# Kernel tuning notes

Measured on AMD Instinct MI355X. Metric: run time of the kernel, lower is better.

Reference implementation:

```python
import jax, jax.numpy as jnp
import numpy as np

B, S, H, NH = 8, 1024, 1024, 16
DH = H // NH


def setup_inputs() -> dict:
    key = jax.random.key(0)
    ks = jax.random.split(key, 16)
    inp = {
        'v': jax.random.normal(ks[0], (B, S, H), jnp.float32),
        'k': jax.random.normal(ks[1], (B, S, H), jnp.float32),
        'q': jax.random.normal(ks[2], (B, S, H), jnp.float32),
        'r': jax.random.normal(ks[3], (B, S, H), jnp.float32),
        'mask': jax.random.randint(ks[4], (B, 1, 1, S), 0, 2).astype(jnp.bool_),
    }
    scale = 1.0 / np.sqrt(H)
    names = ['Wv', 'Wk', 'Wq', 'Wr', 'Wm']
    for i, n in enumerate(names):
        inp[n] = jax.random.normal(ks[5 + i], (H, H), jnp.float32) * scale
        inp['b' + n[1:]] = jnp.zeros((H,), jnp.float32)
    return inp


def _heads(x, W, b):
    # torch Linear: x @ W.T + b, then split heads -> [B, NH, S, DH]
    y = jnp.einsum('bsh,oh->bso', x, W) + b
    return y.reshape(B, S, NH, DH).transpose(0, 2, 1, 3)


def reference(v, k, q, r, mask, Wv, bv, Wk, bk, Wq, bq, Wr, br, Wm, bm):
    vh = _heads(v, Wv, bv)
    kh = _heads(k, Wk, bk)
    qh = _heads(q, Wq, bq)
    rh = _heads(r, Wr, br)
    # relation-augmented scores: (QK^T + RK^T) / sqrt(d_k)
    scores = jnp.einsum('bhqd,bhkd->bhqk', qh + rh, kh) / jnp.sqrt(jnp.asarray(DH, qh.dtype))
    scores = jnp.where(mask, jnp.asarray(-1e9, scores.dtype), scores)
    att = jax.nn.softmax(scores, axis=-1)  # dropout = identity in eval
    out = jnp.einsum('bhqk,bhkd->bhqd', att, vh)
    out = out.transpose(0, 2, 1, 3).reshape(B, S, H)
    return jnp.einsum('bsh,oh->bso', out, Wm) + bm
```

## Files before the change

kernel.cpp:

```cpp
#include <hip/hip_runtime.h>
#include <hip/hip_bf16.h>
#include <stdint.h>

typedef __attribute__((ext_vector_type(4))) float f32x4;
typedef __attribute__((ext_vector_type(8))) short s16x8;
typedef __attribute__((ext_vector_type(4))) short s16x4;

typedef const __attribute__((address_space(1))) unsigned glb_u32;
typedef __attribute__((address_space(3))) unsigned lds_u32;

#define DEVI __device__ __forceinline__

DEVI short f2b(float f) {
    union { float f; unsigned u; } v; v.f = f;
    unsigned r = v.u + 0x7fffu + ((v.u >> 16) & 1u);
    return (short)(r >> 16);
}

struct Ptr5 { const float* p[5]; };
struct Ptr4 { const float* p[4]; };

__global__ __launch_bounds__(256) void cvtW(Ptr5 src, short* __restrict__ dst) {
    const float* s = src.p[blockIdx.y];
    short* d = dst + (size_t)blockIdx.y * (1024u * 1024u);
    int i = (blockIdx.x * 256 + threadIdx.x) * 8;
    f32x4 a = *(const f32x4*)(s + i);
    f32x4 b = *(const f32x4*)(s + i + 4);
    s16x8 o;
#pragma unroll
    for (int j = 0; j < 4; ++j) { o[j] = f2b(a[j]); o[4 + j] = f2b(b[j]); }
    *(s16x8*)(d + i) = o;
}

__global__ __launch_bounds__(256) void cvtA(Ptr4 src, short* __restrict__ dst) {
    const float* s = src.p[blockIdx.y];
    short* d = dst + (size_t)blockIdx.y * (8u * 1024u * 1024u);
    int i = (blockIdx.x * 256 + threadIdx.x) * 8;
    f32x4 a = *(const f32x4*)(s + i);
    f32x4 b = *(const f32x4*)(s + i + 4);
    s16x8 o;
#pragma unroll
    for (int j = 0; j < 4; ++j) { o[j] = f2b(a[j]); o[4 + j] = f2b(b[j]); }
    *(s16x8*)(d + i) = o;
}

template<int AF32, int OUTMODE, int TWO>
__global__ __launch_bounds__(256) void gemm_nt(
    const void* __restrict__ A0_, const void* __restrict__ A1_,
    const short* __restrict__ W0, const short* __restrict__ W1,
    const float* __restrict__ b0, const float* __restrict__ b1,
    void* __restrict__ C_)
{
    constexpr int K = 1024, N = 1024;
    const int tid = threadIdx.x;
    const int lane = tid & 63, wid = tid >> 6;
    const int wm = wid >> 1, wn = wid & 1;
    const int r = lane & 15, g = lane >> 4;

    const int bid = blockIdx.x;
    const int logical = (bid & 7) * 64 + (bid >> 3);
    const int n0 = (logical & 7) * 128, m0 = (logical >> 3) * 128;

    __shared__ alignas(16) short As[2][128 * 32];
    __shared__ alignas(16) short Ws[2][128 * 32];

    auto stage_async = [&](int buf, int kt) {
        int kk = kt * 32;
        const short* Ap = (const short*)A0_; const short* Wp = W0;
        if (TWO && kk >= 1024) { Ap = (const short*)A1_; Wp = W1; kk &= 1023; }
#pragma unroll
        for (int i = 0; i < 2; ++i) {
            int row = wid * 32 + i * 16 + (lane >> 2);
            const short* ga = Ap + (size_t)(m0 + row) * K + kk + (lane & 3) * 8;
            const short* gw = Wp + (size_t)(n0 + row) * K + kk + (lane & 3) * 8;
            __builtin_amdgcn_global_load_lds((glb_u32*)ga,
                (lds_u32*)&As[buf][(wid * 32 + i * 16) * 32], 16, 0, 0);
            __builtin_amdgcn_global_load_lds((glb_u32*)gw,
                (lds_u32*)&Ws[buf][(wid * 32 + i * 16) * 32], 16, 0, 0);
        }
    };

    const int srow = tid >> 1, shalf = tid & 1;
    f32x4 a0g, a1g, a2g, a3g;
    s16x8 wg0, wg1;
    auto load_regs = [&](int kt) {
        int kk = kt * 32;
        const short* wp = W0 + (size_t)(n0 + srow) * K + kk + shalf * 16;
        wg0 = *(const s16x8*)wp;
        wg1 = *(const s16x8*)(wp + 8);
        const float* ap = (const float*)A0_ + (size_t)(m0 + srow) * K + kk + shalf * 16;
        a0g = *(const f32x4*)ap;       a1g = *(const f32x4*)(ap + 4);
        a2g = *(const f32x4*)(ap + 8); a3g = *(const f32x4*)(ap + 12);
    };
    auto store_lds = [&](int buf) {
        s16x8 s0, s1;
#pragma unroll
        for (int j = 0; j < 4; ++j) {
            s0[j] = f2b(a0g[j]); s0[4 + j] = f2b(a1g[j]);
            s1[j] = f2b(a2g[j]); s1[4 + j] = f2b(a3g[j]);
        }
        char* ab = (char*)As[buf];
        *(s16x8*)(ab + srow * 64 + shalf * 32) = s0;
        *(s16x8*)(ab + srow * 64 + shalf * 32 + 16) = s1;
        char* wb = (char*)Ws[buf];
        *(s16x8*)(wb + srow * 64 + shalf * 32) = wg0;
        *(s16x8*)(wb + srow * 64 + shalf * 32 + 16) = wg1;
    };

    f32x4 z = {0.f, 0.f, 0.f, 0.f};
    f32x4 acc[4][4];
#pragma unroll
    for (int i = 0; i < 4; ++i)
#pragma unroll
        for (int j = 0; j < 4; ++j) acc[i][j] = z;

    auto compute = [&](int buf) {
        s16x8 af[4], bfr[4];
#pragma unroll
        for (int f = 0; f < 4; ++f) {
            af[f]  = *(const s16x8*)&As[buf][(wm * 64 + f * 16 + r) * 32 + g * 8];
            bfr[f] = *(const s16x8*)&Ws[buf][(wn * 64 + f * 16 + r) * 32 + g * 8];
        }
#pragma unroll
        for (int i = 0; i < 4; ++i)
#pragma unroll
            for (int j = 0; j < 4; ++j)
                acc[i][j] = __builtin_amdgcn_mfma_f32_16x16x32_bf16(af[i], bfr[j], acc[i][j], 0, 0, 0);
    };

    constexpr int NK = TWO ? 64 : 32;
    if constexpr (AF32) { load_regs(0); store_lds(0); }
    else stage_async(0, 0);
    __syncthreads();
    int buf = 0;
    for (int kt = 0; kt < NK; ++kt) {
        if (kt + 1 < NK) {
            if constexpr (AF32) load_regs(kt + 1);
            else stage_async(buf ^ 1, kt + 1);
        }
        compute(buf);
        if (AF32 && kt + 1 < NK) store_lds(buf ^ 1);
        __syncthreads();
        buf ^= 1;
    }

#pragma unroll
    for (int j = 0; j < 4; ++j) {
        int col = n0 + wn * 64 + j * 16 + r;
        float bb = b0[col];
        if (TWO) bb += b1[col];
#pragma unroll
        for (int i = 0; i < 4; ++i) {
            int rowb = m0 + wm * 64 + i * 16 + g * 4;
            if constexpr (OUTMODE == 2) {
                int bb_ = rowb >> 10, tok = rowb & 1023;
                short* dst = (short*)C_ + ((size_t)(bb_ * 16 + (col >> 6))) * 65536
                           + (size_t)(col & 63) * 1024 + tok;
                s16x4 o;
#pragma unroll
                for (int q = 0; q < 4; ++q) o[q] = f2b(acc[i][j][q] + bb);
                *(s16x4*)dst = o;
            } else {
#pragma unroll
                for (int q = 0; q < 4; ++q) {
                    float val = acc[i][j][q] + bb;
                    if constexpr (OUTMODE == 1)
                        ((float*)C_)[(size_t)(rowb + q) * N + col] = val;
                    else
                        ((short*)C_)[(size_t)(rowb + q) * N + col] = f2b(val);
                }
            }
        }
    }
}

__global__ __launch_bounds__(256) void attn_fwd(
    const short* __restrict__ qrh, const short* __restrict__ kh,
    const short* __restrict__ vT, const int* __restrict__ mask,
    short* __restrict__ outp)
{
    const int bh = blockIdx.x;
    const int b = bh >> 4, h = bh & 15;
    const int qt = blockIdx.y;
    const int tid = threadIdx.x, lane = tid & 63, wid = tid >> 6;
    const int r = lane & 15, g = lane >> 4;

    __shared__ alignas(16) short Ks[64 * 64];
    __shared__ alignas(16) short Vs[64 * 64];
    __shared__ alignas(16) float mb[64];

    const int q0 = qt * 64 + wid * 16;
    const short* qbase = qrh + (size_t)(b * 1024 + q0 + r) * 1024 + h * 64;
    s16x8 qf0 = *(const s16x8*)(qbase + g * 8);
    s16x8 qf1 = *(const s16x8*)(qbase + 32 + g * 8);

    f32x4 z = {0.f, 0.f, 0.f, 0.f};
    f32x4 oacc[4];
#pragma unroll
    for (int i = 0; i < 4; ++i) oacc[i] = z;
    float mrun = -1e30f, lrun = 0.f;

    const int srow = tid >> 2, sq = tid & 3;
    const short* kg = kh + (size_t)(b * 1024 + srow) * 1024 + h * 64 + sq * 16;
    const short* vg = vT + ((size_t)(b * 16 + h)) * 65536 + (size_t)srow * 1024 + sq * 16;
    const int p0s = (sq * 2) ^ (srow & 7), p1s = (sq * 2 + 1) ^ (srow & 7);

    for (int t = 0; t < 16; ++t) {
        const int k0 = t * 64;
        if (t) __syncthreads();
        {
            const short* kp = kg + (size_t)k0 * 1024;
            s16x8 k0v = *(const s16x8*)kp;
            s16x8 k1v = *(const s16x8*)(kp + 8);
            char* kb = (char*)Ks;
            *(s16x8*)(kb + srow * 128 + p0s * 16) = k0v;
            *(s16x8*)(kb + srow * 128 + p1s * 16) = k1v;
        }
        {
            const short* vp = vg + k0;
            s16x8 v0 = *(const s16x8*)vp;
            s16x8 v1 = *(const s16x8*)(vp + 8);
            char* vb = (char*)Vs;
            *(s16x8*)(vb + srow * 128 + p0s * 16) = v0;
            *(s16x8*)(vb + srow * 128 + p1s * 16) = v1;
        }
        if (tid < 64) mb[tid] = mask[b * 1024 + k0 + tid] ? -1e9f : 0.f;
        __syncthreads();

        float p[4][4];
        float tmax = -3e38f;
#pragma unroll
        for (int fn = 0; fn < 4; ++fn) {
            int row = fn * 16 + r;
            char* kb = (char*)Ks;
            s16x8 kfa = *(const s16x8*)(kb + row * 128 + ((g ^ (row & 7)) << 4));
            s16x8 kfb = *(const s16x8*)(kb + row * 128 + (((4 + g) ^ (row & 7)) << 4));
            f32x4 c = __builtin_amdgcn_mfma_f32_16x16x32_bf16(kfa, qf0, z, 0, 0, 0);
            c = __builtin_amdgcn_mfma_f32_16x16x32_bf16(kfb, qf1, c, 0, 0, 0);
            f32x4 mv = *(const f32x4*)&mb[fn * 16 + g * 4];
#pragma unroll
            for (int qi = 0; qi < 4; ++qi) {
                float s = c[qi] * 0.125f + mv[qi];
                p[fn][qi] = s;
                tmax = fmaxf(tmax, s);
            }
        }
        tmax = fmaxf(tmax, __shfl_xor(tmax, 16));
        tmax = fmaxf(tmax, __shfl_xor(tmax, 32));

        float mn = fmaxf(mrun, tmax);
        float corr = __expf(mrun - mn);
        mrun = mn;
        float tsum = 0.f;
#pragma unroll
        for (int fn = 0; fn < 4; ++fn)
#pragma unroll
            for (int qi = 0; qi < 4; ++qi) {
                float e = __expf(p[fn][qi] - mn);
                p[fn][qi] = e;
                tsum += e;
            }
        tsum += __shfl_xor(tsum, 16);
        tsum += __shfl_xor(tsum, 32);
        lrun = lrun * corr + tsum;
#pragma unroll
        for (int df = 0; df < 4; ++df)
#pragma unroll
            for (int qi = 0; qi < 4; ++qi) oacc[df][qi] *= corr;

#pragma unroll
        for (int ks = 0; ks < 2; ++ks) {
            s16x8 pb;
#pragma unroll
            for (int j = 0; j < 4; ++j) {
                pb[j]     = f2b(p[2 * ks][j]);
                pb[4 + j] = f2b(p[2 * ks + 1][j]);
            }
#pragma unroll
            for (int df = 0; df < 4; ++df) {
                int row = df * 16 + r;
                int sl0 = ks * 4 + (g >> 1), half = (g & 1) * 8;
                char* vb = (char*)Vs;
                s16x4 va0 = *(const s16x4*)(vb + row * 128 + ((sl0 ^ (row & 7)) << 4) + half);
                s16x4 va1 = *(const s16x4*)(vb + row * 128 + (((sl0 + 2) ^ (row & 7)) << 4) + half);
                s16x8 vf = {va0[0], va0[1], va0[2], va0[3], va1[0], va1[1], va1[2], va1[3]};
                oacc[df] = __builtin_amdgcn_mfma_f32_16x16x32_bf16(vf, pb, oacc[df], 0, 0, 0);
            }
        }
    }

    float inv = 1.f / lrun;
#pragma unroll
    for (int df = 0; df < 4; ++df) {
        s16x4 o;
#pragma unroll
        for (int qi = 0; qi < 4; ++qi) o[qi] = f2b(oacc[df][qi] * inv);
        *(s16x4*)&outp[(size_t)(b * 1024 + q0 + r) * 1024 + h * 64 + df * 16 + g * 4] = o;
    }
}

extern "C" void kernel_launch(void* const* d_in, const int* in_sizes, int n_in,
                              void* d_out, int out_size, void* d_ws, size_t ws_size,
                              hipStream_t stream) {
    const float* v  = (const float*)d_in[0];
    const float* k  = (const float*)d_in[1];
    const float* q  = (const float*)d_in[2];
    const float* rr = (const float*)d_in[3];
    const int* mask = (const int*)d_in[4];
    const float* Wv = (const float*)d_in[5];  const float* bv = (const float*)d_in[6];
    const float* Wk = (const float*)d_in[7];  const float* bk = (const float*)d_in[8];
    const float* Wq = (const float*)d_in[9];  const float* bq = (const float*)d_in[10];
    const float* Wr = (const float*)d_in[11]; const float* br = (const float*)d_in[12];
    const float* Wm = (const float*)d_in[13]; const float* bm = (const float*)d_in[14];

    const size_t MB = 1048576u;
    const size_t NEED_FULL = 90u * MB;
    const size_t NEED_B    = 74u * MB;
    char* ws = (char*)d_ws;
    short* Wb = (short*)ws;

    Ptr5 p5;
    p5.p[0] = Wv; p5.p[1] = Wk; p5.p[2] = Wq; p5.p[3] = Wr; p5.p[4] = Wm;
    cvtW<<<dim3(512, 5), 256, 0, stream>>>(p5, Wb);

    const short* Wvb = Wb, *Wkb = Wb + 1048576u, *Wqb = Wb + 2097152u,
               *Wrb = Wb + 3145728u, *Wmb = Wb + 4194304u;
    dim3 gg(512);

    if (ws_size >= NEED_FULL) {
        short* vb  = (short*)(ws + 10u * MB);
        short* kb  = vb + 8388608u;
        short* qb  = kb + 8388608u;
        short* rb  = qb + 8388608u;
        short* vtb = rb + 8388608u;
        short* khb = vb;
        short* qrb = kb;
        short* att = qb;

        Ptr4 p4; p4.p[0] = v; p4.p[1] = k; p4.p[2] = q; p4.p[3] = rr;
        cvtA<<<dim3(4096, 4), 256, 0, stream>>>(p4, vb);

        gemm_nt<0, 2, 0><<<gg, 256, 0, stream>>>(vb, nullptr, Wvb, nullptr, bv, nullptr, vtb);
        gemm_nt<0, 0, 0><<<gg, 256, 0, stream>>>(kb, nullptr, Wkb, nullptr, bk, nullptr, khb);
        gemm_nt<0, 0, 1><<<gg, 256, 0, stream>>>(qb, rb, Wqb, Wrb, bq, br, qrb);
        attn_fwd<<<dim3(128, 16), 256, 0, stream>>>(qrb, khb, vtb, mask, att);
        gemm_nt<0, 1, 0><<<gg, 256, 0, stream>>>(att, nullptr, Wmb, nullptr, bm, nullptr, (float*)d_out);
    } else if (ws_size >= NEED_B) {
        short* kb  = (short*)(ws + 10u * MB);
        short* qb  = kb + 8388608u;
        short* rb  = qb + 8388608u;
        short* qrb = rb + 8388608u;
        short* vtb = qb;
        short* khb = rb;
        short* att = kb;

        Ptr4 p4; p4.p[0] = k; p4.p[1] = q; p4.p[2] = rr; p4.p[3] = k;
        cvtA<<<dim3(4096, 3), 256, 0, stream>>>(p4, kb);

        gemm_nt<0, 0, 1><<<gg, 256, 0, stream>>>(qb, rb, Wqb, Wrb, bq, br, qrb);
        gemm_nt<1, 2, 0><<<gg, 256, 0, stream>>>(v, nullptr, Wvb, nullptr, bv, nullptr, vtb);
        gemm_nt<0, 0, 0><<<gg, 256, 0, stream>>>(kb, nullptr, Wkb, nullptr, bk, nullptr, khb);
        attn_fwd<<<dim3(128, 16), 256, 0, stream>>>(qrb, khb, vtb, mask, att);
        gemm_nt<0, 1, 0><<<gg, 256, 0, stream>>>(att, nullptr, Wmb, nullptr, bm, nullptr, (float*)d_out);
    }
}
```

Baseline: 261.1 us.

## Process two query tiles per wave, prefetch K/V tiles, preload full mask

Each wave now handles 32 query rows (two 16-row sub-tiles) so every K and V fragment read from LDS feeds two MFMAs, halving K/V global and LDS traffic per query. The next K/V tile is loaded into registers while the current tile is computed, overlapping global latency with compute. The per-row mask is converted once into a 1024-entry LDS array instead of once per tile. The attention grid is halved to 128x8 blocks, which raises register pressure and lowers the number of blocks available to fill the GPU.

Measured after the change: 253.3 us. 3.0% less time.

```diff
diff --git a/kernel.cpp b/kernel.cpp
--- a/kernel.cpp
+++ b/kernel.cpp
@@ -5,6 +5,7 @@
 typedef __attribute__((ext_vector_type(4))) float f32x4;
 typedef __attribute__((ext_vector_type(8))) short s16x8;
 typedef __attribute__((ext_vector_type(4))) short s16x4;
+typedef __attribute__((ext_vector_type(4))) int i32x4;
 
 typedef const __attribute__((address_space(1))) unsigned glb_u32;
 typedef __attribute__((address_space(3))) unsigned lds_u32;
@@ -187,115 +188,136 @@
 
     __shared__ alignas(16) short Ks[64 * 64];
     __shared__ alignas(16) short Vs[64 * 64];
-    __shared__ alignas(16) float mb[64];
-
-    const int q0 = qt * 64 + wid * 16;
-    const short* qbase = qrh + (size_t)(b * 1024 + q0 + r) * 1024 + h * 64;
-    s16x8 qf0 = *(const s16x8*)(qbase + g * 8);
-    s16x8 qf1 = *(const s16x8*)(qbase + 32 + g * 8);
+    __shared__ alignas(16) float mb[1024];
+
+    {
+        i32x4 mi = *(const i32x4*)(mask + b * 1024 + tid * 4);
+        f32x4 mv;
+#pragma unroll
+        for (int j = 0; j < 4; ++j) mv[j] = mi[j] ? -1e9f : 0.f;
+        *(f32x4*)&mb[tid * 4] = mv;
+    }
+
+    const int q0 = qt * 128 + wid * 32;
+    const short* qbA = qrh + (size_t)(b * 1024 + q0 + r) * 1024 + h * 64;
+    const short* qbB = qbA + 16 * 1024;
+    s16x8 qA0 = *(const s16x8*)(qbA + g * 8);
+    s16x8 qA1 = *(const s16x8*)(qbA + 32 + g * 8);
+    s16x8 qB0 = *(const s16x8*)(qbB + g * 8);
+    s16x8 qB1 = *(const s16x8*)(qbB + 32 + g * 8);
 
     f32x4 z = {0.f, 0.f, 0.f, 0.f};
-    f32x4 oacc[4];
-#pragma unroll
-    for (int i = 0; i < 4; ++i) oacc[i] = z;
-    float mrun = -1e30f, lrun = 0.f;
+    f32x4 oA[4], oB[4];
+#pragma unroll
+    for (int i = 0; i < 4; ++i) { oA[i] = z; oB[i] = z; }
+    float mA = -1e30f, mB = -1e30f, lA = 0.f, lB = 0.f;
 
     const int srow = tid >> 2, sq = tid & 3;
     const short* kg = kh + (size_t)(b * 1024 + srow) * 1024 + h * 64 + sq * 16;
     const short* vg = vT + ((size_t)(b * 16 + h)) * 65536 + (size_t)srow * 1024 + sq * 16;
     const int p0s = (sq * 2) ^ (srow & 7), p1s = (sq * 2 + 1) ^ (srow & 7);
 
+    s16x8 kr0, kr1, vr0, vr1;
+    auto stage_load = [&](int t) {
+        const short* kp = kg + (size_t)(t * 64) * 1024;
+        kr0 = *(const s16x8*)kp; kr1 = *(const s16x8*)(kp + 8);
+        const short* vp = vg + t * 64;
+        vr0 = *(const s16x8*)vp; vr1 = *(const s16x8*)(vp + 8);
+    };
+    auto stage_write = [&]() {
+        char* kb2 = (char*)Ks;
+        *(s16x8*)(kb2 + srow * 128 + p0s * 16) = kr0;
+        *(s16x8*)(kb2 + srow * 128 + p1s * 16) = kr1;
+        char* vb2 = (char*)Vs;
+        *(s16x8*)(vb2 + srow * 128 + p0s * 16) = vr0;
+        *(s16x8*)(vb2 + srow * 128 + p1s * 16) = vr1;
+    };
+
+    stage_load(0);
     for (int t = 0; t < 16; ++t) {
-        const int k0 = t * 64;
         if (t) __syncthreads();
-        {
-            const short* kp = kg + (size_t)k0 * 1024;
-            s16x8 k0v = *(const s16x8*)kp;
-            s16x8 k1v = *(const s16x8*)(kp + 8);
-            char* kb = (char*)Ks;
-            *(s16x8*)(kb + srow * 128 + p0s * 16) = k0v;
-            *(s16x8*)(kb + srow * 128 + p1s * 16) = k1v;
-        }
-        {
-            const short* vp = vg + k0;
-            s16x8 v0 = *(const s16x8*)vp;
-            s16x8 v1 = *(const s16x8*)(vp + 8);
-            char* vb = (char*)Vs;
-            *(s16x8*)(vb + srow * 128 + p0s * 16) = v0;
-            *(s16x8*)(vb + srow * 128 + p1s * 16) = v1;
-        }
-        if (tid < 64) mb[tid] = mask[b * 1024 + k0 + tid] ? -1e9f : 0.f;
+        stage_write();
         __syncthreads();
-
-        float p[4][4];
-        float tmax = -3e38f;
+        if (t < 15) stage_load(t + 1);
+
+        f32x4 pA[4], pB[4];
+        float tmA = -3e38f, tmB = -3e38f;
+        char* kb2 = (char*)Ks;
 #pragma unroll
         for (int fn = 0; fn < 4; ++fn) {
             int row = fn * 16 + r;
-            char* kb = (char*)Ks;
-            s16x8 kfa = *(const s16x8*)(kb + row * 128 + ((g ^ (row & 7)) << 4));
-            s16x8 kfb = *(const s16x8*)(kb + row * 128 + (((4 + g) ^ (row & 7)) << 4));
-            f32x4 c = __builtin_amdgcn_mfma_f32_16x16x32_bf16(kfa, qf0, z, 0, 0, 0);
-            c = __builtin_amdgcn_mfma_f32_16x16x32_bf16(kfb, qf1, c, 0, 0, 0);
-            f32x4 mv = *(const f32x4*)&mb[fn * 16 + g * 4];
+            s16x8 kfa = *(const s16x8*)(kb2 + row * 128 + ((g ^ (row & 7)) << 4));
+            s16x8 kfb = *(const s16x8*)(kb2 + row * 128 + (((4 + g) ^ (row & 7)) << 4));
+            f32x4 cA = __builtin_amdgcn_mfma_f32_16x16x32_bf16(kfa, qA0, z, 0, 0, 0);
+            cA = __builtin_amdgcn_mfma_f32_16x16x32_bf16(kfb, qA1, cA, 0, 0, 0);
+            f32x4 cB = __builtin_amdgcn_mfma_f32_16x16x32_bf16(kfa, qB0, z, 0, 0, 0);
+            cB = __builtin_amdgcn_mfma_f32_16x16x32_bf16(kfb, qB1, cB, 0, 0, 0);
+            f32x4 mv = *(const f32x4*)&mb[t * 64 + fn * 16 + g * 4];
 #pragma unroll
             for (int qi = 0; qi < 4; ++qi) {
-                float s = c[qi] * 0.125f + mv[qi];
-                p[fn][qi] = s;
-                tmax = fmaxf(tmax, s);
-            }
-        }
-        tmax = fmaxf(tmax, __shfl_xor(tmax, 16));
-        tmax = fmaxf(tmax, __shfl_xor(tmax, 32));
-
-        float mn = fmaxf(mrun, tmax);
-        float corr = __expf(mrun - mn);
-        mrun = mn;
-        float tsum = 0.f;
+                float sA = cA[qi] * 0.125f + mv[qi];
+                float sB = cB[qi] * 0.125f + mv[qi];
+                pA[fn][qi] = sA; pB[fn][qi] = sB;
+                tmA = fmaxf(tmA, sA); tmB = fmaxf(tmB, sB);
+            }
+        }
+        tmA = fmaxf(tmA, __shfl_xor(tmA, 16)); tmA = fmaxf(tmA, __shfl_xor(tmA, 32));
+        tmB = fmaxf(tmB, __shfl_xor(tmB, 16)); tmB = fmaxf(tmB, __shfl_xor(tmB, 32));
+
+        float mnA = fmaxf(mA, tmA), mnB = fmaxf(mB, tmB);
+        float cA_ = __expf(mA - mnA), cB_ = __expf(mB - mnB);
+        mA = mnA; mB = mnB;
+        float tsA = 0.f, tsB = 0.f;
 #pragma unroll
         for (int fn = 0; fn < 4; ++fn)
 #pragma unroll
             for (int qi = 0; qi < 4; ++qi) {
-                float e = __expf(p[fn][qi] - mn);
-                p[fn][qi] = e;
-                tsum += e;
-            }
-        tsum += __shfl_xor(tsum, 16);
-        tsum += __shfl_xor(tsum, 32);
-        lrun = lrun * corr + tsum;
+                float eA = __expf(pA[fn][qi] - mA); pA[fn][qi] = eA; tsA += eA;
+                float eB = __expf(pB[fn][qi] - mB); pB[fn][qi] = eB; tsB += eB;
+            }
+        tsA += __shfl_xor(tsA, 16); tsA += __shfl_xor(tsA, 32);
+        tsB += __shfl_xor(tsB, 16); tsB += __shfl_xor(tsB, 32);
+        lA = lA * cA_ + tsA; lB = lB * cB_ + tsB;
 #pragma unroll
         for (int df = 0; df < 4; ++df)
 #pragma unroll
-            for (int qi = 0; qi < 4; ++qi) oacc[df][qi] *= corr;
-
+            for (int qi = 0; qi < 4; ++qi) { oA[df][qi] *= cA_; oB[df][qi] *= cB_; }
+
+        char* vb2 = (char*)Vs;
 #pragma unroll
         for (int ks = 0; ks < 2; ++ks) {
-            s16x8 pb;
+            s16x8 pbA, pbB;
 #pragma unroll
             for (int j = 0; j < 4; ++j) {
-                pb[j]     = f2b(p[2 * ks][j]);
-                pb[4 + j] = f2b(p[2 * ks + 1][j]);
+                pbA[j]     = f2b(pA[2 * ks][j]);
+                pbA[4 + j] = f2b(pA[2 * ks + 1][j]);
+                pbB[j]     = f2b(pB[2 * ks][j]);
+                pbB[4 + j] = f2b(pB[2 * ks + 1][j]);
             }
 #pragma unroll
             for (int df = 0; df < 4; ++df) {
                 int row = df * 16 + r;
                 int sl0 = ks * 4 + (g >> 1), half = (g & 1) * 8;
-                char* vb = (char*)Vs;
-                s16x4 va0 = *(const s16x4*)(vb + row * 128 + ((sl0 ^ (row & 7)) << 4) + half);
-                s16x4 va1 = *(const s16x4*)(vb + row * 128 + (((sl0 + 2) ^ (row & 7)) << 4) + half);
+                s16x4 va0 = *(const s16x4*)(vb2 + row * 128 + ((sl0 ^ (row & 7)) << 4) + half);
+                s16x4 va1 = *(const s16x4*)(vb2 + row * 128 + (((sl0 + 2) ^ (row & 7)) << 4) + half);
                 s16x8 vf = {va0[0], va0[1], va0[2], va0[3], va1[0], va1[1], va1[2], va1[3]};
-                oacc[df] = __builtin_amdgcn_mfma_f32_16x16x32_bf16(vf, pb, oacc[df], 0, 0, 0);
-            }
-        }
-    }
-
-    float inv = 1.f / lrun;
+                oA[df] = __builtin_amdgcn_mfma_f32_16x16x32_bf16(vf, pbA, oA[df], 0, 0, 0);
+                oB[df] = __builtin_amdgcn_mfma_f32_16x16x32_bf16(vf, pbB, oB[df], 0, 0, 0);
+            }
+        }
+    }
+
+    float ivA = 1.f / lA, ivB = 1.f / lB;
 #pragma unroll
     for (int df = 0; df < 4; ++df) {
-        s16x4 o;
-#pragma unroll
-        for (int qi = 0; qi < 4; ++qi) o[qi] = f2b(oacc[df][qi] * inv);
-        *(s16x4*)&outp[(size_t)(b * 1024 + q0 + r) * 1024 + h * 64 + df * 16 + g * 4] = o;
+        s16x4 oa, ob;
+#pragma unroll
+        for (int qi = 0; qi < 4; ++qi) {
+            oa[qi] = f2b(oA[df][qi] * ivA);
+            ob[qi] = f2b(oB[df][qi] * ivB);
+        }
+        *(s16x4*)&outp[(size_t)(b * 1024 + q0 + r) * 1024 + h * 64 + df * 16 + g * 4] = oa;
+        *(s16x4*)&outp[(size_t)(b * 1024 + q0 + 16 + r) * 1024 + h * 64 + df * 16 + g * 4] = ob;
     }
 }
 
@@ -343,7 +365,7 @@
         gemm_nt<0, 2, 0><<<gg, 256, 0, stream>>>(vb, nullptr, Wvb, nullptr, bv, nullptr, vtb);
         gemm_nt<0, 0, 0><<<gg, 256, 0, stream>>>(kb, nullptr, Wkb, nullptr, bk, nullptr, khb);
         gemm_nt<0, 0, 1><<<gg, 256, 0, stream>>>(qb, rb, Wqb, Wrb, bq, br, qrb);
-        attn_fwd<<<dim3(128, 16), 256, 0, stream>>>(qrb, khb, vtb, mask, att);
+        attn_fwd<<<dim3(128, 8), 256, 0, stream>>>(qrb, khb, vtb, mask, att);
         gemm_nt<0, 1, 0><<<gg, 256, 0, stream>>>(att, nullptr, Wmb, nullptr, bm, nullptr, (float*)d_out);
     } else if (ws_size >= NEED_B) {
         short* kb  = (short*)(ws + 10u * MB);
@@ -360,7 +382,7 @@
         gemm_nt<0, 0, 1><<<gg, 256, 0, stream>>>(qb, rb, Wqb, Wrb, bq, br, qrb);
         gemm_nt<1, 2, 0><<<gg, 256, 0, stream>>>(v, nullptr, Wvb, nullptr, bv, nullptr, vtb);
         gemm_nt<0, 0, 0><<<gg, 256, 0, stream>>>(kb, nullptr, Wkb, nullptr, bk, nullptr, khb);
-        attn_fwd<<<dim3(128, 16), 256, 0, stream>>>(qrb, khb, vtb, mask, att);
+        attn_fwd<<<dim3(128, 8), 256, 0, stream>>>(qrb, khb, vtb, mask, att);
         gemm_nt<0, 1, 0><<<gg, 256, 0, stream>>>(att, nullptr, Wmb, nullptr, bm, nullptr, (float*)d_out);
     }
 }
```
